# Kernel tuning notes

Measured on AMD Instinct MI355X. Metric: run time of the kernel, lower is better.

Reference implementation:

```python
import jax, jax.numpy as jnp
import numpy as np

# Semantic hierarchy configuration (stand-in for semantic_softmax_processor)
GROUP_SIZES = [8192, 4096, 2048, 1024, 512, 256, 128, 64, 32, 16]
NORM_FACTORS = [0.1] * len(GROUP_SIZES)
TOPK_CAP = 500
TEMPERATURE = 1.0
TOTAL_CLASSES = sum(GROUP_SIZES)  # 16368
BATCH = 1024


def setup_inputs() -> dict:
    key = jax.random.key(0)
    k1, k2, k3 = jax.random.split(key, 3)
    logits = jax.random.normal(k1, (BATCH, TOTAL_CLASSES), dtype=jnp.float32)
    logits_teacher = jax.random.normal(k2, (BATCH, TOTAL_CLASSES), dtype=jnp.float32)
    targets = jax.random.randint(k3, (BATCH,), 0, TOTAL_CLASSES, dtype=jnp.int64)
    return {"logits": logits, "logits_teacher": logits_teacher, "targets": targets}


def _group_kd_loss(s_logits, t_logits, temperature):
    # s_logits, t_logits: [B, C_i] for one semantic group
    B, C = t_logits.shape
    k = min(C, TOPK_CAP)
    # teacher top-k classes (sorted, largest)
    t_top, t_idx = jax.lax.top_k(t_logits, k)                 # [B, k]
    s_top = jnp.take_along_axis(s_logits, t_idx, axis=1)      # [B, k]
    log_p = jax.nn.log_softmax(s_top / temperature, axis=1)   # student log-probs
    log_q = jax.nn.log_softmax(t_top / temperature, axis=1)   # teacher log-probs
    q = jnp.exp(log_q)
    # KL(q || p), reduction='batchmean'
    kl = jnp.sum(q * (log_q - log_p)) / B
    return kl * temperature * temperature


def reference(logits, logits_teacher, targets):
    # targets are converted to semantic targets in the original module but are
    # never used in the loss computation (dead code) -> no effect on output.
    del targets
    total = jnp.float32(0.0)
    offset = 0
    for gsize, norm in zip(GROUP_SIZES, NORM_FACTORS):
        s_i = jax.lax.slice_in_dim(logits, offset, offset + gsize, axis=1)
        t_i = jax.lax.slice_in_dim(logits_teacher, offset, offset + gsize, axis=1)
        total = total + _group_kd_loss(s_i, t_i, TEMPERATURE) * norm
        offset += gsize
    return total
```

## Files before the change

### kernel.cpp

```cpp
#include <hip/hip_runtime.h>
#include <stdint.h>
#include <float.h>

#define TOTAL 16368
#define KSEL 500
#define CAP 1536
#define NSLOT 24
#define NBUCKET 64

__device__ __forceinline__ uint32_t fkey(float f) {
    uint32_t u = __float_as_uint(f);
    return (u & 0x80000000u) ? ~u : (u | 0x80000000u);
}
__device__ __forceinline__ float keyf(uint32_t k) {
    uint32_t u = (k & 0x80000000u) ? (k & 0x7FFFFFFFu) : ~k;
    return __uint_as_float(u);
}

__device__ __forceinline__ int wave_sumi(int v) {
    #pragma unroll
    for (int o = 32; o > 0; o >>= 1) v += __shfl_xor(v, o, 64);
    return v;
}
__device__ __forceinline__ float wave_sumf(float v) {
    #pragma unroll
    for (int o = 32; o > 0; o >>= 1) v += __shfl_xor(v, o, 64);
    return v;
}
__device__ __forceinline__ float wave_maxf(float v) {
    #pragma unroll
    for (int o = 32; o > 0; o >>= 1) v = fmaxf(v, __shfl_xor(v, o, 64));
    return v;
}

__device__ __forceinline__ void lse_merge(float& m, float& l, float m2, float l2) {
    float M = fmaxf(m, m2);
    l = l * __expf(m - M) + l2 * __expf(m2 - M);
    m = M;
}

__device__ __noinline__ void wave_slow_kl(const float* __restrict__ t,
                                          const float* __restrict__ s, int C,
                                          float* __restrict__ partial) {
    const int lane = threadIdx.x & 63;
    uint64_t lo = 0ull, hi = (1ull << 45), tau = 0ull;
    int cl = C, ch = 0;
    for (int it = 0; it < 100; ++it) {
        uint64_t span = hi - lo;
        if (span <= 1ull) { tau = lo; break; }
        uint64_t mid;
        if (it & 1) mid = lo + (span >> 1);
        else {
            uint64_t st = span * (uint64_t)(cl - KSEL) / (uint64_t)(cl - ch);
            if (st < 1) st = 1;
            if (st > span - 1) st = span - 1;
            mid = lo + st;
        }
        int c = 0;
        for (int i = lane; i < C; i += 64) {
            uint64_t ck = ((uint64_t)fkey(t[i]) << 13) | (uint64_t)(8191 - i);
            c += (ck > mid);
        }
        c = wave_sumi(c);
        if (c == KSEL) { tau = mid; break; }
        if (c > KSEL) { lo = mid; cl = c; } else { hi = mid; ch = c; }
    }
    float tmx = -FLT_MAX;
    for (int i = lane; i < C; i += 64) tmx = fmaxf(tmx, t[i]);
    tmx = wave_maxf(tmx);
    float St = 0.f, Stt = 0.f, Sts = 0.f, sm = -FLT_MAX;
    for (int i = lane; i < C; i += 64) {
        float x = t[i];
        uint64_t ck = ((uint64_t)fkey(x) << 13) | (uint64_t)(8191 - i);
        if (ck > tau) {
            float e = __expf(x - tmx), v = s[i];
            St += e; Stt += e * x; Sts += e * v;
            sm = fmaxf(sm, v);
        }
    }
    St = wave_sumf(St); Stt = wave_sumf(Stt); Sts = wave_sumf(Sts); sm = wave_maxf(sm);
    float Ss = 0.f;
    for (int i = lane; i < C; i += 64) {
        uint64_t ck = ((uint64_t)fkey(t[i]) << 13) | (uint64_t)(8191 - i);
        if (ck > tau) Ss += __expf(s[i] - sm);
    }
    Ss = wave_sumf(Ss);
    if (lane == 0) {
        float kl = (Stt - Sts) / St - tmx - __logf(St) + sm + __logf(Ss);
        atomicAdd(partial, kl * (0.1f / 1024.f));
    }
}

template <int NS, class IdxF>
__device__ void select_accum(uint32_t (&key)[NS], int nValid, IdxF idxOf,
                             const float* __restrict__ s, float* __restrict__ partial) {
    const int lane = threadIdx.x & 63;
    uint32_t kmx = 0u, kmn = 0xFFFFFFFFu;
    #pragma unroll
    for (int j = 0; j < NS; ++j) {
        uint32_t k = key[j];
        kmx = k > kmx ? k : kmx;
        if (k) kmn = k < kmn ? k : kmn;
    }
    #pragma unroll
    for (int o = 32; o > 0; o >>= 1) {
        uint32_t a = __shfl_xor(kmx, o, 64); kmx = a > kmx ? a : kmx;
        uint32_t b = __shfl_xor(kmn, o, 64); kmn = b < kmn ? b : kmn;
    }
    const float tmax = keyf(kmx);

    uint32_t tauhi; int cut;
    if (nValid == KSEL) { tauhi = kmn - 1u; cut = -1; }
    else {
        uint32_t lo = kmn - 1u, hi = kmx;
        int cl = nValid, ch = 0;
        bool exact = false;
        tauhi = hi; cut = -1;
        for (int it = 0; it < 80; ++it) {
            uint32_t span = hi - lo;
            if (span <= 1u) break;
            uint32_t mid;
            if (!(it & 1)) {
                uint64_t st = (uint64_t)span * (uint32_t)(cl - KSEL) / (uint32_t)(cl - ch);
                if (st < 1) st = 1;
                if (st > span - 1) st = span - 1;
                mid = lo + (uint32_t)st;
            } else mid = lo + (span >> 1);
            int c = 0;
            #pragma unroll
            for (int j = 0; j < NS; ++j) c += (key[j] > mid);
            c = wave_sumi(c);
            if (c == KSEL) { tauhi = mid; cut = -1; exact = true; break; }
            if (c > KSEL) { lo = mid; cl = c; } else { hi = mid; ch = c; }
        }
        if (!exact) {
            tauhi = hi;
            const int nT = KSEL - ch, nTie = cl - ch;
            if (nT >= nTie) cut = 0x7FFFFFFF;
            else {
                int l = -1, h = 8191;
                while (h - l > 1) {
                    int m = (l + h) >> 1;
                    int c = 0;
                    #pragma unroll
                    for (int j = 0; j < NS; ++j)
                        c += (key[j] == tauhi && idxOf(j) <= m);
                    c = wave_sumi(c);
                    if (c >= nT) h = m; else l = m;
                }
                cut = h;
            }
        }
    }

    uint32_t selm = 0u;
    float sv[NS];
    #pragma unroll
    for (int j = 0; j < NS; ++j) {
        uint32_t kj = key[j];
        bool sj = (kj > tauhi) || (kj == tauhi && idxOf(j) <= cut);
        selm |= (sj ? 1u : 0u) << j;
        sv[j] = sj ? s[idxOf(j)] : 0.f;
    }
    float St = 0.f, Stt = 0.f, Sts = 0.f, sm = -FLT_MAX;
    #pragma unroll
    for (int j = 0; j < NS; ++j) {
        if (selm & (1u << j)) {
            float tv = keyf(key[j]);
            float e = __expf(tv - tmax);
            St += e; Stt += e * tv; Sts += e * sv[j];
            sm = fmaxf(sm, sv[j]);
        }
    }
    #pragma unroll
    for (int o = 32; o > 0; o >>= 1) {
        St  += __shfl_xor(St,  o, 64);
        Stt += __shfl_xor(Stt, o, 64);
        Sts += __shfl_xor(Sts, o, 64);
        sm = fmaxf(sm, __shfl_xor(sm, o, 64));
    }
    float Ss = 0.f;
    #pragma unroll
    for (int j = 0; j < NS; ++j)
        if (selm & (1u << j)) Ss += __expf(sv[j] - sm);
    Ss = wave_sumf(Ss);
    if (lane == 0) {
        float kl = (Stt - Sts) / St - tmax - __logf(St) + sm + __logf(Ss);
        atomicAdd(partial, kl * (0.1f / 1024.f));
    }
}

template <int NJ>
__device__ void mid_wave(const float* __restrict__ t, const float* __restrict__ s,
                         float* __restrict__ partial) {
    const int lane = threadIdx.x & 63;
    const float4* t4 = (const float4*)t;
    uint32_t key[NJ];
    #pragma unroll
    for (int c = 0; c < NJ / 4; ++c) {
        float4 x = t4[lane + c * 64];
        key[4 * c + 0] = fkey(x.x); key[4 * c + 1] = fkey(x.y);
        key[4 * c + 2] = fkey(x.z); key[4 * c + 3] = fkey(x.w);
    }
    auto idxOf = [&](int j) { return ((lane + (j >> 2) * 64) << 2) + (j & 3); };
    select_accum<NJ>(key, NJ * 64, idxOf, s, partial);
}

template <int NJ4>
__device__ void big_wave(const float* __restrict__ t, const float* __restrict__ s,
                         float thr, float* __restrict__ partial,
                         float* vals, uint16_t* idxs) {
    const int lane = threadIdx.x & 63;
    const float4* t4 = (const float4*)t;
    const uint64_t ltm = (1ull << lane) - 1ull;
    int cnt = 0;
    #pragma unroll
    for (int c0 = 0; c0 < NJ4; c0 += 8) {
        float4 buf[8];
        #pragma unroll
        for (int u = 0; u < 8; ++u) buf[u] = t4[(c0 + u) * 64 + lane];
        #pragma unroll
        for (int u = 0; u < 8; ++u) {
            float xs[4] = {buf[u].x, buf[u].y, buf[u].z, buf[u].w};
            #pragma unroll
            for (int q = 0; q < 4; ++q) {
                bool p = xs[q] > thr;
                uint64_t mb = __ballot(p);
                if (p) {
                    int pos = cnt + (int)__popcll(mb & ltm);
                    if (pos < CAP) {
                        vals[pos] = xs[q];
                        idxs[pos] = (uint16_t)((((c0 + u) * 64 + lane) << 2) + q);
                    }
                }
                cnt += (int)__popcll(mb);
            }
        }
    }
    if (cnt < KSEL || cnt > CAP) { wave_slow_kl(t, s, NJ4 * 256, partial); return; }
    uint32_t key[NSLOT], gidx[NSLOT];
    #pragma unroll
    for (int j = 0; j < NSLOT; ++j) {
        int p = lane + j * 64;
        bool v = p < cnt;
        key[j]  = v ? fkey(vals[p]) : 0u;
        gidx[j] = v ? (uint32_t)idxs[p] : 0u;
    }
    auto idxOf = [&](int j) { return (int)gidx[j]; };
    select_accum<NSLOT>(key, cnt, idxOf, s, partial);
}

__device__ void tiny_group(const float* __restrict__ t, const float* __restrict__ s,
                           int Cg, float* __restrict__ partial) {
    const int lane = threadIdx.x & 63;
    float St = 0.f, Stt = 0.f, Sts = 0.f, m = -FLT_MAX, l = 0.f;
    float tv[4], svv[4];
    #pragma unroll
    for (int q = 0; q < 4; ++q) {
        int i = lane + q * 64;
        bool va = i < Cg;
        tv[q] = va ? t[i] : -FLT_MAX;
        svv[q] = va ? s[i] : 0.f;
    }
    float mx = -FLT_MAX;
    #pragma unroll
    for (int q = 0; q < 4; ++q) mx = fmaxf(mx, tv[q]);
    mx = wave_maxf(mx);
    #pragma unroll
    for (int q = 0; q < 4; ++q) {
        if (lane + q * 64 < Cg) {
            float e = __expf(tv[q] - mx);
            St += e; Stt += e * tv[q]; Sts += e * svv[q];
            float x = svv[q];
            if (x > m) { l = l * __expf(m - x) + 1.f; m = x; }
            else       { l += __expf(x - m); }
        }
    }
    #pragma unroll
    for (int o = 32; o > 0; o >>= 1) {
        St  += __shfl_xor(St,  o, 64);
        Stt += __shfl_xor(Stt, o, 64);
        Sts += __shfl_xor(Sts, o, 64);
        float m2 = __shfl_xor(m, o, 64);
        float l2 = __shfl_xor(l, o, 64);
        lse_merge(m, l, m2, l2);
    }
    if (lane == 0) {
        float kl = (Stt - Sts) / St - mx - __logf(St) + m + __logf(l);
        atomicAdd(partial, kl * (0.1f / 1024.f));
    }
}

__global__ __launch_bounds__(64, 4) void kd_all(const float* __restrict__ sL,
                                                const float* __restrict__ tL,
                                                float* __restrict__ partial) {
    __shared__ float    vals[CAP];
    __shared__ uint16_t idxs[CAP];
    const int row = blockIdx.x;
    const int y = blockIdx.y;
    const float* tr = tL + (size_t)row * TOTAL;
    const float* sr = sL + (size_t)row * TOTAL;
    float* p = partial + ((row + y * 37) & (NBUCKET - 1));

    switch (y) {
    case 0: big_wave<32>(tr, sr, 1.10f, p, vals, idxs); break;
    case 1: big_wave<16>(tr + 8192, sr + 8192, 0.60f, p, vals, idxs); break;
    case 2:
        mid_wave<32>(tr + 12288, sr + 12288, p);
        mid_wave<16>(tr + 14336, sr + 14336, p);
        break;
    default:
        mid_wave<8>(tr + 15360, sr + 15360, p);
        tiny_group(tr + 15872, sr + 15872, 256, p);
        tiny_group(tr + 16128, sr + 16128, 128, p);
        tiny_group(tr + 16256, sr + 16256, 64, p);
        tiny_group(tr + 16320, sr + 16320, 32, p);
        tiny_group(tr + 16352, sr + 16352, 16, p);
        break;
    }
}

__global__ void zero_ws(float* partial) {
    if (threadIdx.x < NBUCKET) partial[threadIdx.x] = 0.f;
}

__global__ void final_sum(const float* __restrict__ partial, float* __restrict__ out) {
    float v = (threadIdx.x < NBUCKET) ? partial[threadIdx.x] : 0.f;
    #pragma unroll
    for (int o = 32; o > 0; o >>= 1) v += __shfl_down(v, o, 64);
    if (threadIdx.x == 0) out[0] = v;
}

extern "C" void kernel_launch(void* const* d_in, const int* in_sizes, int n_in,
                              void* d_out, int out_size, void* d_ws, size_t ws_size,
                              hipStream_t stream) {
    (void)in_sizes; (void)n_in; (void)ws_size; (void)out_size;
    const float* s = (const float*)d_in[0];
    const float* t = (const float*)d_in[1];
    float* out = (float*)d_out;
    float* partial = (float*)d_ws;

    hipLaunchKernelGGL(zero_ws, dim3(1), dim3(64), 0, stream, partial);
    hipLaunchKernelGGL(kd_all, dim3(1024, 4), dim3(64), 0, stream, s, t, partial);
    hipLaunchKernelGGL(final_sum, dim3(1), dim3(64), 0, stream, partial, out);
}
```

Measured before the change: 193.9 us.

## Stage teacher rows into LDS via async global_load_lds and drop atomics

Teacher slices for the large and mid groups are now copied into a 32KB LDS staging buffer with global_load_lds DMA before scanning. Mid-group student values are prefetched unconditionally, so their loads no longer wait on the selection mask. Per-block results go to distinct workspace slots when the workspace is large enough, which removes the zero kernel and the atomics, and the final reduction grows to 256 threads. The larger shared allocation lowers how many blocks fit on each CU, and the launch-bounds occupancy hint is removed.

```diff
diff --git a/kernel.cpp b/kernel.cpp
--- a/kernel.cpp
+++ b/kernel.cpp
@@ -32,16 +32,20 @@
     for (int o = 32; o > 0; o >>= 1) v = fmaxf(v, __shfl_xor(v, o, 64));
     return v;
 }
-
 __device__ __forceinline__ void lse_merge(float& m, float& l, float m2, float l2) {
     float M = fmaxf(m, m2);
     l = l * __expf(m - M) + l2 * __expf(m2 - M);
     m = M;
 }
 
-__device__ __noinline__ void wave_slow_kl(const float* __restrict__ t,
-                                          const float* __restrict__ s, int C,
-                                          float* __restrict__ partial) {
+__device__ __forceinline__ void dma16(const void* g, void* l) {
+    __builtin_amdgcn_global_load_lds(
+        (const __attribute__((address_space(1))) void*)g,
+        (__attribute__((address_space(3))) void*)l, 16, 0, 0);
+}
+
+__device__ __noinline__ float wave_slow_kl(const float* __restrict__ t,
+                                           const float* __restrict__ s, int C) {
     const int lane = threadIdx.x & 63;
     uint64_t lo = 0ull, hi = (1ull << 45), tau = 0ull;
     int cl = C, ch = 0;
@@ -85,16 +89,20 @@
         if (ck > tau) Ss += __expf(s[i] - sm);
     }
     Ss = wave_sumf(Ss);
-    if (lane == 0) {
-        float kl = (Stt - Sts) / St - tmx - __logf(St) + sm + __logf(Ss);
-        atomicAdd(partial, kl * (0.1f / 1024.f));
-    }
-}
-
-template <int NS, class IdxF>
-__device__ void select_accum(uint32_t (&key)[NS], int nValid, IdxF idxOf,
-                             const float* __restrict__ s, float* __restrict__ partial) {
-    const int lane = threadIdx.x & 63;
+    if (lane == 0)
+        return (Stt - Sts) / St - tmx - __logf(St) + sm + __logf(Ss);
+    return 0.f;
+}
+
+template <int NS, bool PREF, class IdxF>
+__device__ float select_accum(uint32_t (&key)[NS], int nValid, IdxF idxOf,
+                              const float* __restrict__ s) {
+    const int lane = threadIdx.x & 63;
+    float svp[NS];
+    if (PREF) {
+        #pragma unroll
+        for (int j = 0; j < NS; ++j) svp[j] = s[idxOf(j)];
+    }
     uint32_t kmx = 0u, kmn = 0xFFFFFFFFu;
     #pragma unroll
     for (int j = 0; j < NS; ++j) {
@@ -160,7 +168,7 @@
         uint32_t kj = key[j];
         bool sj = (kj > tauhi) || (kj == tauhi && idxOf(j) <= cut);
         selm |= (sj ? 1u : 0u) << j;
-        sv[j] = sj ? s[idxOf(j)] : 0.f;
+        sv[j] = PREF ? svp[j] : (sj ? s[idxOf(j)] : 0.f);
     }
     float St = 0.f, Stt = 0.f, Sts = 0.f, sm = -FLT_MAX;
     #pragma unroll
@@ -184,41 +192,29 @@
     for (int j = 0; j < NS; ++j)
         if (selm & (1u << j)) Ss += __expf(sv[j] - sm);
     Ss = wave_sumf(Ss);
-    if (lane == 0) {
-        float kl = (Stt - Sts) / St - tmax - __logf(St) + sm + __logf(Ss);
-        atomicAdd(partial, kl * (0.1f / 1024.f));
-    }
-}
-
-template <int NJ>
-__device__ void mid_wave(const float* __restrict__ t, const float* __restrict__ s,
-                         float* __restrict__ partial) {
-    const int lane = threadIdx.x & 63;
-    const float4* t4 = (const float4*)t;
-    uint32_t key[NJ];
-    #pragma unroll
-    for (int c = 0; c < NJ / 4; ++c) {
-        float4 x = t4[lane + c * 64];
-        key[4 * c + 0] = fkey(x.x); key[4 * c + 1] = fkey(x.y);
-        key[4 * c + 2] = fkey(x.z); key[4 * c + 3] = fkey(x.w);
-    }
-    auto idxOf = [&](int j) { return ((lane + (j >> 2) * 64) << 2) + (j & 3); };
-    select_accum<NJ>(key, NJ * 64, idxOf, s, partial);
-}
-
-template <int NJ4>
-__device__ void big_wave(const float* __restrict__ t, const float* __restrict__ s,
-                         float thr, float* __restrict__ partial,
-                         float* vals, uint16_t* idxs) {
-    const int lane = threadIdx.x & 63;
-    const float4* t4 = (const float4*)t;
+    if (lane == 0)
+        return (Stt - Sts) / St - tmax - __logf(St) + sm + __logf(Ss);
+    return 0.f;
+}
+
+template <int NCH>
+__device__ float big_wave(const float* __restrict__ tg, const float* __restrict__ s,
+                          float thr, float* stageF, uint16_t* idxs) {
+    const int lane = threadIdx.x & 63;
+    #pragma unroll
+    for (int c = 0; c < NCH; ++c)
+        dma16((const char*)tg + c * 1024 + lane * 16, (char*)stageF + c * 1024);
+    asm volatile("s_waitcnt vmcnt(0)" ::: "memory");
+
+    const float4* st4 = (const float4*)stageF;
+    float* vals = stageF;
     const uint64_t ltm = (1ull << lane) - 1ull;
     int cnt = 0;
     #pragma unroll
-    for (int c0 = 0; c0 < NJ4; c0 += 8) {
+    for (int c0 = 0; c0 < NCH * 64; c0 += 512) {
         float4 buf[8];
         #pragma unroll
-        for (int u = 0; u < 8; ++u) buf[u] = t4[(c0 + u) * 64 + lane];
+        for (int u = 0; u < 8; ++u) buf[u] = st4[c0 + u * 64 + lane];
         #pragma unroll
         for (int u = 0; u < 8; ++u) {
             float xs[4] = {buf[u].x, buf[u].y, buf[u].z, buf[u].w};
@@ -230,14 +226,14 @@
                     int pos = cnt + (int)__popcll(mb & ltm);
                     if (pos < CAP) {
                         vals[pos] = xs[q];
-                        idxs[pos] = (uint16_t)((((c0 + u) * 64 + lane) << 2) + q);
+                        idxs[pos] = (uint16_t)(((c0 + u * 64 + lane) << 2) + q);
                     }
                 }
                 cnt += (int)__popcll(mb);
             }
         }
     }
-    if (cnt < KSEL || cnt > CAP) { wave_slow_kl(t, s, NJ4 * 256, partial); return; }
+    if (cnt < KSEL || cnt > CAP) return wave_slow_kl(tg, s, NCH * 256);
     uint32_t key[NSLOT], gidx[NSLOT];
     #pragma unroll
     for (int j = 0; j < NSLOT; ++j) {
@@ -247,11 +243,26 @@
         gidx[j] = v ? (uint32_t)idxs[p] : 0u;
     }
     auto idxOf = [&](int j) { return (int)gidx[j]; };
-    select_accum<NSLOT>(key, cnt, idxOf, s, partial);
-}
-
-__device__ void tiny_group(const float* __restrict__ t, const float* __restrict__ s,
-                           int Cg, float* __restrict__ partial) {
+    return select_accum<NSLOT, false>(key, cnt, idxOf, s);
+}
+
+template <int NJ>
+__device__ float mid_wave(const float* __restrict__ t, const float* __restrict__ s) {
+    const int lane = threadIdx.x & 63;
+    const float4* t4 = (const float4*)t;
+    uint32_t key[NJ];
+    #pragma unroll
+    for (int c = 0; c < NJ / 4; ++c) {
+        float4 x = t4[lane + c * 64];
+        key[4 * c + 0] = fkey(x.x); key[4 * c + 1] = fkey(x.y);
+        key[4 * c + 2] = fkey(x.z); key[4 * c + 3] = fkey(x.w);
+    }
+    auto idxOf = [&](int j) { return ((lane + (j >> 2) * 64) << 2) + (j & 3); };
+    return select_accum<NJ, true>(key, NJ * 64, idxOf, s);
+}
+
+__device__ float tiny_group(const float* __restrict__ t, const float* __restrict__ s,
+                            int Cg) {
     const int lane = threadIdx.x & 63;
     float St = 0.f, Stt = 0.f, Sts = 0.f, m = -FLT_MAX, l = 0.f;
     float tv[4], svv[4];
@@ -285,38 +296,49 @@
         float l2 = __shfl_xor(l, o, 64);
         lse_merge(m, l, m2, l2);
     }
-    if (lane == 0) {
-        float kl = (Stt - Sts) / St - mx - __logf(St) + m + __logf(l);
-        atomicAdd(partial, kl * (0.1f / 1024.f));
-    }
-}
-
-__global__ __launch_bounds__(64, 4) void kd_all(const float* __restrict__ sL,
-                                                const float* __restrict__ tL,
-                                                float* __restrict__ partial) {
-    __shared__ float    vals[CAP];
+    if (lane == 0)
+        return (Stt - Sts) / St - mx - __logf(St) + m + __logf(l);
+    return 0.f;
+}
+
+__global__ __launch_bounds__(64) void kd_all(const float* __restrict__ sL,
+                                             const float* __restrict__ tL,
+                                             float* __restrict__ res, int mode) {
+    __shared__ float    stageF[8192];
     __shared__ uint16_t idxs[CAP];
     const int row = blockIdx.x;
     const int y = blockIdx.y;
     const float* tr = tL + (size_t)row * TOTAL;
     const float* sr = sL + (size_t)row * TOTAL;
-    float* p = partial + ((row + y * 37) & (NBUCKET - 1));
-
+    const int lane = threadIdx.x & 63;
+
+    float kl = 0.f;
     switch (y) {
-    case 0: big_wave<32>(tr, sr, 1.10f, p, vals, idxs); break;
-    case 1: big_wave<16>(tr + 8192, sr + 8192, 0.60f, p, vals, idxs); break;
-    case 2:
-        mid_wave<32>(tr + 12288, sr + 12288, p);
-        mid_wave<16>(tr + 14336, sr + 14336, p);
+    case 0: kl = big_wave<32>(tr,        sr,        1.10f, stageF, idxs); break;
+    case 1: kl = big_wave<16>(tr + 8192, sr + 8192, 0.60f, stageF, idxs); break;
+    case 2: {
+        #pragma unroll
+        for (int c = 0; c < 12; ++c)
+            dma16((const char*)(tr + 12288) + c * 1024 + lane * 16,
+                  (char*)stageF + c * 1024);
+        asm volatile("s_waitcnt vmcnt(0)" ::: "memory");
+        kl  = mid_wave<32>(stageF,        sr + 12288);
+        kl += mid_wave<16>(stageF + 2048, sr + 14336);
         break;
+    }
     default:
-        mid_wave<8>(tr + 15360, sr + 15360, p);
-        tiny_group(tr + 15872, sr + 15872, 256, p);
-        tiny_group(tr + 16128, sr + 16128, 128, p);
-        tiny_group(tr + 16256, sr + 16256, 64, p);
-        tiny_group(tr + 16320, sr + 16320, 32, p);
-        tiny_group(tr + 16352, sr + 16352, 16, p);
+        kl  = mid_wave<8>(tr + 15360, sr + 15360);
+        kl += tiny_group(tr + 15872, sr + 15872, 256);
+        kl += tiny_group(tr + 16128, sr + 16128, 128);
+        kl += tiny_group(tr + 16256, sr + 16256, 64);
+        kl += tiny_group(tr + 16320, sr + 16320, 32);
+        kl += tiny_group(tr + 16352, sr + 16352, 16);
         break;
+    }
+    if (lane == 0) {
+        float v = kl * (0.1f / 1024.f);
+        if (mode) res[row * 4 + y] = v;
+        else atomicAdd(&res[(row + y * 37) & (NBUCKET - 1)], v);
     }
 }
 
@@ -324,23 +346,30 @@
     if (threadIdx.x < NBUCKET) partial[threadIdx.x] = 0.f;
 }
 
-__global__ void final_sum(const float* __restrict__ partial, float* __restrict__ out) {
-    float v = (threadIdx.x < NBUCKET) ? partial[threadIdx.x] : 0.f;
+__global__ void final_sum(const float* __restrict__ partial, float* __restrict__ out,
+                          int n) {
+    __shared__ float scr[4];
+    float v = 0.f;
+    for (int i = threadIdx.x; i < n; i += 256) v += partial[i];
     #pragma unroll
     for (int o = 32; o > 0; o >>= 1) v += __shfl_down(v, o, 64);
-    if (threadIdx.x == 0) out[0] = v;
+    if ((threadIdx.x & 63) == 0) scr[threadIdx.x >> 6] = v;
+    __syncthreads();
+    if (threadIdx.x == 0) out[0] = scr[0] + scr[1] + scr[2] + scr[3];
 }
 
 extern "C" void kernel_launch(void* const* d_in, const int* in_sizes, int n_in,
                               void* d_out, int out_size, void* d_ws, size_t ws_size,
                               hipStream_t stream) {
-    (void)in_sizes; (void)n_in; (void)ws_size; (void)out_size;
+    (void)in_sizes; (void)n_in; (void)out_size;
     const float* s = (const float*)d_in[0];
     const float* t = (const float*)d_in[1];
     float* out = (float*)d_out;
-    float* partial = (float*)d_ws;
-
-    hipLaunchKernelGGL(zero_ws, dim3(1), dim3(64), 0, stream, partial);
-    hipLaunchKernelGGL(kd_all, dim3(1024, 4), dim3(64), 0, stream, s, t, partial);
-    hipLaunchKernelGGL(final_sum, dim3(1), dim3(64), 0, stream, partial, out);
-}
+    float* ws = (float*)d_ws;
+
+    const int mode = (ws_size >= 4096 * sizeof(float)) ? 1 : 0;
+    if (!mode) hipLaunchKernelGGL(zero_ws, dim3(1), dim3(64), 0, stream, ws);
+    hipLaunchKernelGGL(kd_all, dim3(1024, 4), dim3(64), 0, stream, s, t, ws, mode);
+    hipLaunchKernelGGL(final_sum, dim3(1), dim3(256), 0, stream, ws, out,
+                       mode ? 4096 : NBUCKET);
+}
```

Result: slower. 204.6 us (+5.5%).
